# Optimization experiments

Hardware: AMD Instinct MI355X
Metric: run time of the kernel (lower is better)

Reference implementation:

```python
import jax, jax.numpy as jnp
import numpy as np

N_NODES = 100000  # graph size (set via set_features/adj_lists in the original)
DEGREE = 32       # sampled neighbors per node (num_sample)
N_PAIRS = 8192    # link-prediction batch
FEAT_DIM = 9      # nn.Embedding(18, 9)
HID = 20          # enc1 embed_dim
OUT = 15          # n_out / enc2 embed_dim


def setup_inputs() -> dict:
    key = jax.random.key(0)
    ks = jax.random.split(key, 9)
    to_pred = jax.random.randint(ks[0], (N_PAIRS, 2), 0, N_NODES)
    adj = jax.random.randint(ks[1], (N_NODES, DEGREE), 0, N_NODES)
    feat = jax.random.normal(ks[2], (N_NODES, FEAT_DIM), dtype=jnp.float32)
    W1 = jax.random.normal(ks[3], (HID, 2 * FEAT_DIM), dtype=jnp.float32) * 0.1
    W2 = jax.random.normal(ks[4], (OUT, HID), dtype=jnp.float32) * 0.1
    fc1_w = jax.random.normal(ks[5], (15, 30), dtype=jnp.float32) * 0.1
    fc1_b = jnp.zeros((15,), dtype=jnp.float32)
    fc2_w = jax.random.normal(ks[6], (1, 15), dtype=jnp.float32) * 0.1
    fc2_b = jnp.zeros((1,), dtype=jnp.float32)
    return {"to_pred": to_pred, "adj": adj, "feat": feat, "W1": W1, "W2": W2,
            "fc1_w": fc1_w, "fc1_b": fc1_b, "fc2_w": fc2_w, "fc2_b": fc2_b}


def _enc1(nodes, feat, adj, W1):
    # GraphSAGE layer 1 (gcn=False): concat(self, mean(neighbors)) -> relu(W1 @ .)
    neigh_feat = feat[adj[nodes]].mean(axis=-2)          # [..., FEAT_DIM]
    combined = jnp.concatenate([feat[nodes], neigh_feat], axis=-1)  # [..., 2*FEAT_DIM]
    return jax.nn.relu(combined @ W1.T)                  # [..., HID]


def _enc2(nodes, feat, adj, W1, W2):
    # GraphSAGE layer 2 (gcn=True): neighbor set includes self, mean-only aggregate
    neighs = jnp.concatenate([adj[nodes], nodes[:, None]], axis=-1)  # [B, K+1]
    h1 = _enc1(neighs, feat, adj, W1)                    # [B, K+1, HID]
    return jax.nn.relu(h1.mean(axis=1) @ W2.T)           # [B, OUT]


def reference(to_pred, adj, feat, W1, W2, fc1_w, fc1_b, fc2_w, fc2_b):
    # two_fc_link_prediction: embed both endpoints, concat, 2-layer ReLU MLP
    e1 = _enc2(to_pred[:, 0], feat, adj, W1, W2)         # [B, OUT]
    e2 = _enc2(to_pred[:, 1], feat, adj, W1, W2)         # [B, OUT]
    cat = jnp.concatenate([e1, e2], axis=1)              # [B, 30]
    h = jax.nn.relu(cat @ fc1_w.T + fc1_b)               # [B, 15]
    out = jax.nn.relu(h @ fc2_w.T + fc2_b)               # [B, 1]
    return jnp.squeeze(out, axis=-1)                     # [B]
```

## Files before the change

### kernel.cpp

```cpp
#include <hip/hip_runtime.h>
#include <hip/hip_bf16.h>

#define N_NODES 100000
#define DEGREE 32
#define N_PAIRS 8192
#define FEAT 9
#define HID 20
#define NOUT 15
#define FPAD 16

#define NPB 28
#define PPB 8

__global__ __launch_bounds__(256) void k_prep(
    const float* __restrict__ feat, __hip_bfloat16* __restrict__ featb) {
  int e = blockIdx.x * 256 + threadIdx.x;
  if (e < N_NODES * FPAD) {
    int row = e >> 4;
    int col = e & (FPAD - 1);
    float v = (col < FEAT) ? feat[row * FEAT + col] : 0.f;
    featb[e] = __float2bfloat16(v);
  }
}

__global__ __launch_bounds__(256) void k_node_all(
    const int* __restrict__ adj,
    const float* __restrict__ feat,
    const __hip_bfloat16* __restrict__ featb,
    const float* __restrict__ W1,
    const float* __restrict__ W2,
    __hip_bfloat16* __restrict__ t_ws) {
  __shared__ float sW1[HID * 2 * FEAT];
  __shared__ float sW2[NOUT * HID];
  __shared__ float sComb[NPB][2 * FEAT];
  __shared__ float sH[NPB][HID];

  int tid = threadIdx.x;
  for (int i = tid; i < HID * 2 * FEAT; i += 256) sW1[i] = W1[i];
  for (int i = tid; i < NOUT * HID; i += 256) sW2[i] = W2[i];

  int base = blockIdx.x * NPB;

  if (tid < NPB * FEAT) {
    int nl = tid / FEAT;
    int j = tid - nl * FEAT;
    int n = base + nl;
    if (n < N_NODES) {
      const int4* arow4 = (const int4*)(adj + n * DEGREE);
      float s = 0.f;
#pragma unroll
      for (int c = 0; c < DEGREE / 4; ++c) {
        int4 a4 = arow4[c];
        s += __bfloat162float(featb[a4.x * FPAD + j]);
        s += __bfloat162float(featb[a4.y * FPAD + j]);
        s += __bfloat162float(featb[a4.z * FPAD + j]);
        s += __bfloat162float(featb[a4.w * FPAD + j]);
      }
      sComb[nl][j] = feat[n * FEAT + j];
      sComb[nl][FEAT + j] = s * (1.0f / DEGREE);
    }
  }
  __syncthreads();

  for (int idx = tid; idx < NPB * HID; idx += 256) {
    int nl = idx / HID;
    int i = idx - nl * HID;
    if (base + nl < N_NODES) {
      float acc = 0.f;
#pragma unroll
      for (int j = 0; j < 2 * FEAT; ++j) acc += sW1[i * 2 * FEAT + j] * sComb[nl][j];
      sH[nl][i] = fmaxf(acc, 0.f);
    }
  }
  __syncthreads();

  for (int idx = tid; idx < NPB * NOUT; idx += 256) {
    int nl = idx / NOUT;
    int d = idx - nl * NOUT;
    int n = base + nl;
    if (n < N_NODES) {
      float acc = 0.f;
#pragma unroll
      for (int i = 0; i < HID; ++i) acc += sW2[d * HID + i] * sH[nl][i];
      t_ws[n * FPAD + d] = __float2bfloat16(acc);
    }
  }
}

__global__ __launch_bounds__(256) void k_pair_all(
    const int* __restrict__ to_pred,
    const int* __restrict__ adj,
    const __hip_bfloat16* __restrict__ t_ws,
    const float* __restrict__ fc1_w,
    const float* __restrict__ fc1_b,
    const float* __restrict__ fc2_w,
    const float* __restrict__ fc2_b,
    float* __restrict__ out) {
  __shared__ float s1[15 * 30];
  __shared__ float b1v[15];
  __shared__ float s2v[15];
  __shared__ float b2v;
  __shared__ float sE[PPB][30];
  __shared__ float sHh[PPB][15];

  int tid = threadIdx.x;
  for (int i = tid; i < 15 * 30; i += 256) s1[i] = fc1_w[i];
  if (tid < 15) {
    b1v[tid] = fc1_b[tid];
    s2v[tid] = fc2_w[tid];
  }
  if (tid == 0) b2v = fc2_b[0];

  int pbase = blockIdx.x * PPB;

  if (tid < PPB * 30) {
    int pl = tid / 30;
    int slot = tid - pl * 30;
    int side = slot / 15;
    int d = slot - side * 15;
    int p = pbase + pl;
    int node = to_pred[2 * p + side];
    const int4* arow4 = (const int4*)(adj + node * DEGREE);
    float s = __bfloat162float(t_ws[node * FPAD + d]);
#pragma unroll
    for (int c = 0; c < DEGREE / 4; ++c) {
      int4 a4 = arow4[c];
      s += __bfloat162float(t_ws[a4.x * FPAD + d]);
      s += __bfloat162float(t_ws[a4.y * FPAD + d]);
      s += __bfloat162float(t_ws[a4.z * FPAD + d]);
      s += __bfloat162float(t_ws[a4.w * FPAD + d]);
    }
    sE[pl][slot] = fmaxf(s * (1.0f / (DEGREE + 1)), 0.f);
  }
  __syncthreads();

  if (tid < PPB * 15) {
    int pl = tid / 15;
    int i = tid - pl * 15;
    float acc = b1v[i];
#pragma unroll
    for (int j = 0; j < 30; ++j) acc += s1[i * 30 + j] * sE[pl][j];
    sHh[pl][i] = fmaxf(acc, 0.f);
  }
  __syncthreads();

  if (tid < PPB) {
    float acc = b2v;
#pragma unroll
    for (int i = 0; i < 15; ++i) acc += s2v[i] * sHh[tid][i];
    out[pbase + tid] = fmaxf(acc, 0.f);
  }
}

extern "C" void kernel_launch(void* const* d_in, const int* in_sizes, int n_in,
                              void* d_out, int out_size, void* d_ws,
                              size_t ws_size, hipStream_t stream) {
  const int* to_pred = (const int*)d_in[0];
  const int* adj     = (const int*)d_in[1];
  const float* feat  = (const float*)d_in[2];
  const float* W1    = (const float*)d_in[3];
  const float* W2    = (const float*)d_in[4];
  const float* fc1_w = (const float*)d_in[5];
  const float* fc1_b = (const float*)d_in[6];
  const float* fc2_w = (const float*)d_in[7];
  const float* fc2_b = (const float*)d_in[8];
  float* out         = (float*)d_out;

  __hip_bfloat16* featb = (__hip_bfloat16*)d_ws;
  __hip_bfloat16* t_ws  = featb + (size_t)N_NODES * FPAD;

  int grid0 = (N_NODES * FPAD + 255) / 256;
  k_prep<<<grid0, 256, 0, stream>>>(feat, featb);

  int grid1 = (N_NODES + NPB - 1) / NPB;
  k_node_all<<<grid1, 256, 0, stream>>>(adj, feat, featb, W1, W2, t_ws);

  int grid2 = N_PAIRS / PPB;
  k_pair_all<<<grid2, 256, 0, stream>>>(to_pred, adj, t_ws, fc1_w, fc1_b,
                                        fc2_w, fc2_b, out);
}
```

Measured before the change: 119.2 us.

## Fuse prep, node and pair kernels into one cooperative persistent kernel

Replaces three separate kernel launches with a single cooperative kernel whose blocks loop over work chunks, separated by grid-wide syncs between the feature conversion, node-embedding and pair-MLP phases. The feature bf16 conversion now has one thread per node write two 16-byte vectors instead of one thread per element. This targets launch overhead and inter-kernel gaps, at the cost of grid.sync barriers and a persistent grid sized from occupancy (assumes 256 CUs), which may underfill or imbalance the gather-heavy phases.

```diff
diff --git a/kernel.cpp b/kernel.cpp
--- a/kernel.cpp
+++ b/kernel.cpp
@@ -1,5 +1,8 @@
 #include <hip/hip_runtime.h>
 #include <hip/hip_bf16.h>
+#include <hip/hip_cooperative_groups.h>
+
+namespace cg = cooperative_groups;
 
 #define N_NODES 100000
 #define DEGREE 32
@@ -11,91 +14,26 @@
 
 #define NPB 28
 #define PPB 8
-
-__global__ __launch_bounds__(256) void k_prep(
-    const float* __restrict__ feat, __hip_bfloat16* __restrict__ featb) {
-  int e = blockIdx.x * 256 + threadIdx.x;
-  if (e < N_NODES * FPAD) {
-    int row = e >> 4;
-    int col = e & (FPAD - 1);
-    float v = (col < FEAT) ? feat[row * FEAT + col] : 0.f;
-    featb[e] = __float2bfloat16(v);
-  }
-}
-
-__global__ __launch_bounds__(256) void k_node_all(
+#define NCHUNK_B ((N_NODES + NPB - 1) / NPB)
+#define NCHUNK_C (N_PAIRS / PPB)
+
+__global__ __launch_bounds__(256, 4) void k_fused(
+    const int* __restrict__ to_pred,
     const int* __restrict__ adj,
     const float* __restrict__ feat,
-    const __hip_bfloat16* __restrict__ featb,
     const float* __restrict__ W1,
     const float* __restrict__ W2,
-    __hip_bfloat16* __restrict__ t_ws) {
+    const float* __restrict__ fc1_w,
+    const float* __restrict__ fc1_b,
+    const float* __restrict__ fc2_w,
+    const float* __restrict__ fc2_b,
+    __hip_bfloat16* __restrict__ featb,
+    __hip_bfloat16* __restrict__ t_ws,
+    float* __restrict__ out) {
   __shared__ float sW1[HID * 2 * FEAT];
   __shared__ float sW2[NOUT * HID];
   __shared__ float sComb[NPB][2 * FEAT];
   __shared__ float sH[NPB][HID];
-
-  int tid = threadIdx.x;
-  for (int i = tid; i < HID * 2 * FEAT; i += 256) sW1[i] = W1[i];
-  for (int i = tid; i < NOUT * HID; i += 256) sW2[i] = W2[i];
-
-  int base = blockIdx.x * NPB;
-
-  if (tid < NPB * FEAT) {
-    int nl = tid / FEAT;
-    int j = tid - nl * FEAT;
-    int n = base + nl;
-    if (n < N_NODES) {
-      const int4* arow4 = (const int4*)(adj + n * DEGREE);
-      float s = 0.f;
-#pragma unroll
-      for (int c = 0; c < DEGREE / 4; ++c) {
-        int4 a4 = arow4[c];
-        s += __bfloat162float(featb[a4.x * FPAD + j]);
-        s += __bfloat162float(featb[a4.y * FPAD + j]);
-        s += __bfloat162float(featb[a4.z * FPAD + j]);
-        s += __bfloat162float(featb[a4.w * FPAD + j]);
-      }
-      sComb[nl][j] = feat[n * FEAT + j];
-      sComb[nl][FEAT + j] = s * (1.0f / DEGREE);
-    }
-  }
-  __syncthreads();
-
-  for (int idx = tid; idx < NPB * HID; idx += 256) {
-    int nl = idx / HID;
-    int i = idx - nl * HID;
-    if (base + nl < N_NODES) {
-      float acc = 0.f;
-#pragma unroll
-      for (int j = 0; j < 2 * FEAT; ++j) acc += sW1[i * 2 * FEAT + j] * sComb[nl][j];
-      sH[nl][i] = fmaxf(acc, 0.f);
-    }
-  }
-  __syncthreads();
-
-  for (int idx = tid; idx < NPB * NOUT; idx += 256) {
-    int nl = idx / NOUT;
-    int d = idx - nl * NOUT;
-    int n = base + nl;
-    if (n < N_NODES) {
-      float acc = 0.f;
-#pragma unroll
-      for (int i = 0; i < HID; ++i) acc += sW2[d * HID + i] * sH[nl][i];
-      t_ws[n * FPAD + d] = __float2bfloat16(acc);
-    }
-  }
-}
-
-__global__ __launch_bounds__(256) void k_pair_all(
-    const int* __restrict__ to_pred,
-    const int* __restrict__ adj,
-    const __hip_bfloat16* __restrict__ t_ws,
-    const float* __restrict__ fc1_w,
-    const float* __restrict__ fc1_b,
-    const float* __restrict__ fc2_w,
-    const float* __restrict__ fc2_b,
-    float* __restrict__ out) {
   __shared__ float s1[15 * 30];
   __shared__ float b1v[15];
   __shared__ float s2v[15];
@@ -104,51 +42,124 @@
   __shared__ float sHh[PPB][15];
 
   int tid = threadIdx.x;
+  for (int i = tid; i < HID * 2 * FEAT; i += 256) sW1[i] = W1[i];
+  for (int i = tid; i < NOUT * HID; i += 256) sW2[i] = W2[i];
   for (int i = tid; i < 15 * 30; i += 256) s1[i] = fc1_w[i];
   if (tid < 15) {
     b1v[tid] = fc1_b[tid];
     s2v[tid] = fc2_w[tid];
   }
   if (tid == 0) b2v = fc2_b[0];
-
-  int pbase = blockIdx.x * PPB;
-
-  if (tid < PPB * 30) {
-    int pl = tid / 30;
-    int slot = tid - pl * 30;
-    int side = slot / 15;
-    int d = slot - side * 15;
-    int p = pbase + pl;
-    int node = to_pred[2 * p + side];
-    const int4* arow4 = (const int4*)(adj + node * DEGREE);
-    float s = __bfloat162float(t_ws[node * FPAD + d]);
-#pragma unroll
-    for (int c = 0; c < DEGREE / 4; ++c) {
-      int4 a4 = arow4[c];
-      s += __bfloat162float(t_ws[a4.x * FPAD + d]);
-      s += __bfloat162float(t_ws[a4.y * FPAD + d]);
-      s += __bfloat162float(t_ws[a4.z * FPAD + d]);
-      s += __bfloat162float(t_ws[a4.w * FPAD + d]);
-    }
-    sE[pl][slot] = fmaxf(s * (1.0f / (DEGREE + 1)), 0.f);
-  }
   __syncthreads();
 
-  if (tid < PPB * 15) {
-    int pl = tid / 15;
-    int i = tid - pl * 15;
-    float acc = b1v[i];
-#pragma unroll
-    for (int j = 0; j < 30; ++j) acc += s1[i * 30 + j] * sE[pl][j];
-    sHh[pl][i] = fmaxf(acc, 0.f);
-  }
-  __syncthreads();
-
-  if (tid < PPB) {
-    float acc = b2v;
-#pragma unroll
-    for (int i = 0; i < 15; ++i) acc += s2v[i] * sHh[tid][i];
-    out[pbase + tid] = fmaxf(acc, 0.f);
+  cg::grid_group grid = cg::this_grid();
+
+  for (int n = blockIdx.x * 256 + tid; n < N_NODES; n += gridDim.x * 256) {
+    const float* fr = feat + (size_t)n * FEAT;
+    __hip_bfloat16 u[FPAD];
+#pragma unroll
+    for (int j = 0; j < FEAT; ++j) u[j] = __float2bfloat16(fr[j]);
+#pragma unroll
+    for (int j = FEAT; j < FPAD; ++j) u[j] = __float2bfloat16(0.f);
+    uint4* dst = (uint4*)(featb + (size_t)n * FPAD);
+    dst[0] = *(const uint4*)(u);
+    dst[1] = *(const uint4*)(u + 8);
+  }
+  grid.sync();
+
+  for (int c = blockIdx.x; c < NCHUNK_B; c += gridDim.x) {
+    int base = c * NPB;
+
+    if (tid < NPB * FEAT) {
+      int nl = tid / FEAT;
+      int j = tid - nl * FEAT;
+      int n = base + nl;
+      if (n < N_NODES) {
+        const int4* arow4 = (const int4*)(adj + (size_t)n * DEGREE);
+        float s = 0.f;
+#pragma unroll
+        for (int cc = 0; cc < DEGREE / 4; ++cc) {
+          int4 a4 = arow4[cc];
+          s += __bfloat162float(featb[a4.x * FPAD + j]);
+          s += __bfloat162float(featb[a4.y * FPAD + j]);
+          s += __bfloat162float(featb[a4.z * FPAD + j]);
+          s += __bfloat162float(featb[a4.w * FPAD + j]);
+        }
+        sComb[nl][j] = feat[(size_t)n * FEAT + j];
+        sComb[nl][FEAT + j] = s * (1.0f / DEGREE);
+      }
+    }
+    __syncthreads();
+
+    for (int idx = tid; idx < NPB * HID; idx += 256) {
+      int nl = idx / HID;
+      int i = idx - nl * HID;
+      if (base + nl < N_NODES) {
+        float acc = 0.f;
+#pragma unroll
+        for (int j = 0; j < 2 * FEAT; ++j)
+          acc += sW1[i * 2 * FEAT + j] * sComb[nl][j];
+        sH[nl][i] = fmaxf(acc, 0.f);
+      }
+    }
+    __syncthreads();
+
+    for (int idx = tid; idx < NPB * NOUT; idx += 256) {
+      int nl = idx / NOUT;
+      int d = idx - nl * NOUT;
+      int n = base + nl;
+      if (n < N_NODES) {
+        float acc = 0.f;
+#pragma unroll
+        for (int i = 0; i < HID; ++i) acc += sW2[d * HID + i] * sH[nl][i];
+        t_ws[(size_t)n * FPAD + d] = __float2bfloat16(acc);
+      }
+    }
+    __syncthreads();
+  }
+  grid.sync();
+
+  for (int c = blockIdx.x; c < NCHUNK_C; c += gridDim.x) {
+    int pbase = c * PPB;
+
+    if (tid < PPB * 30) {
+      int pl = tid / 30;
+      int slot = tid - pl * 30;
+      int side = slot / 15;
+      int d = slot - side * 15;
+      int p = pbase + pl;
+      int node = to_pred[2 * p + side];
+      const int4* arow4 = (const int4*)(adj + (size_t)node * DEGREE);
+      float s = __bfloat162float(t_ws[node * FPAD + d]);
+#pragma unroll
+      for (int cc = 0; cc < DEGREE / 4; ++cc) {
+        int4 a4 = arow4[cc];
+        s += __bfloat162float(t_ws[a4.x * FPAD + d]);
+        s += __bfloat162float(t_ws[a4.y * FPAD + d]);
+        s += __bfloat162float(t_ws[a4.z * FPAD + d]);
+        s += __bfloat162float(t_ws[a4.w * FPAD + d]);
+      }
+      sE[pl][slot] = fmaxf(s * (1.0f / (DEGREE + 1)), 0.f);
+    }
+    __syncthreads();
+
+    if (tid < PPB * 15) {
+      int pl = tid / 15;
+      int i = tid - pl * 15;
+      float acc = b1v[i];
+#pragma unroll
+      for (int j = 0; j < 30; ++j) acc += s1[i * 30 + j] * sE[pl][j];
+      sHh[pl][i] = fmaxf(acc, 0.f);
+    }
+    __syncthreads();
+
+    if (tid < PPB) {
+      float acc = b2v;
+#pragma unroll
+      for (int i = 0; i < 15; ++i) acc += s2v[i] * sHh[tid][i];
+      out[pbase + tid] = fmaxf(acc, 0.f);
+    }
+    __syncthreads();
   }
 }
 
@@ -169,13 +180,21 @@
   __hip_bfloat16* featb = (__hip_bfloat16*)d_ws;
   __hip_bfloat16* t_ws  = featb + (size_t)N_NODES * FPAD;
 
-  int grid0 = (N_NODES * FPAD + 255) / 256;
-  k_prep<<<grid0, 256, 0, stream>>>(feat, featb);
-
-  int grid1 = (N_NODES + NPB - 1) / NPB;
-  k_node_all<<<grid1, 256, 0, stream>>>(adj, feat, featb, W1, W2, t_ws);
-
-  int grid2 = N_PAIRS / PPB;
-  k_pair_all<<<grid2, 256, 0, stream>>>(to_pred, adj, t_ws, fc1_w, fc1_b,
-                                        fc2_w, fc2_b, out);
+  static int coop_grid = 0;
+  if (coop_grid == 0) {
+    int nb = 0;
+    hipOccupancyMaxActiveBlocksPerMultiprocessor(
+        &nb, reinterpret_cast<const void*>(k_fused), 256, 0);
+    if (nb < 1) nb = 1;
+    if (nb > 8) nb = 8;
+    coop_grid = nb * 256;
+  }
+
+  void* params[] = {
+      (void*)&to_pred, (void*)&adj, (void*)&feat, (void*)&W1, (void*)&W2,
+      (void*)&fc1_w, (void*)&fc1_b, (void*)&fc2_w, (void*)&fc2_b,
+      (void*)&featb, (void*)&t_ws, (void*)&out};
+
+  hipLaunchCooperativeKernel(reinterpret_cast<const void*>(k_fused),
+                             dim3(coop_grid), dim3(256), params, 0, stream);
 }
```

Measured after the change: 286.8 us. +140.7%, slower.
